# Performance work log

Hardware: AMD Instinct MI355X
Metric: run time of the kernel (lower is better)

Reference implementation:

```python
import jax, jax.numpy as jnp
import numpy as np

V = 400000
D = 16  # max_degree
EPS = 1e-6


def setup_inputs() -> dict:
    key = jax.random.key(0)
    k1, k2, k3, k4 = jax.random.split(key, 4)
    new_verts_coords = jax.random.normal(k1, (V, 3), dtype=jnp.float32)
    verts_src = jax.random.normal(k2, (V, 3), dtype=jnp.float32)
    neighborhood_indices = jax.random.randint(k3, (V, D), 0, V, dtype=jnp.int64)
    neighborhood_weights = jax.random.uniform(k4, (V, D), dtype=jnp.float32)
    return {
        "new_verts_coords": new_verts_coords,
        "verts_src": verts_src,
        "neighborhood_indices": neighborhood_indices,
        "neighborhood_weights": neighborhood_weights,
    }


def reference(new_verts_coords, verts_src, neighborhood_indices, neighborhood_weights):
    # Gather neighbor coords and center at each vertex: (V, D, 3)
    nb_src = verts_src[neighborhood_indices] - verts_src[:, None, :]
    nb_trg = new_verts_coords[neighborhood_indices] - new_verts_coords[:, None, :]

    # Per-vertex cross-covariance 3x3 (Procrustes), regularized as in original
    XtY = jnp.einsum('vdi,vdj->vij', nb_src, nb_trg) + EPS * jnp.eye(3, dtype=nb_src.dtype)

    # Batched tiny SVD; torch.svd returns V (not V^T), R_iT = V @ U^T = (U @ Vh)^T
    U, S, Vh = jnp.linalg.svd(XtY)
    R_iT = jnp.swapaxes(U @ Vh, -1, -2)  # (V, 3, 3)

    # Rotate source neighborhoods and compare to target: (V, D, 3)
    Y_hat = jnp.einsum('vdi,vij->vdj', nb_src, R_iT)
    diff = jnp.linalg.norm(Y_hat - nb_trg, axis=-1)  # (V, D)

    loss_rigid = (diff * neighborhood_weights).sum() / (neighborhood_weights.sum() + EPS)
    return loss_rigid
```

## Files before the change

kernel.cpp:

```cpp
#include <hip/hip_runtime.h>
#include <hip/hip_fp16.h>
#include <math.h>

#define NV   400000
#define DEG  16
#define BLK  256
#define NBLK ((NV + BLK - 1) / BLK)

#define PARTS_OFF  0
#define PACKED_OFF 16384

typedef int   iv4 __attribute__((ext_vector_type(4)));
typedef float fv4 __attribute__((ext_vector_type(4)));
typedef unsigned int uv3 __attribute__((ext_vector_type(3)));

__device__ __forceinline__ float2 h2f2(unsigned int u) {
    union { unsigned int u; __half2 h; } c; c.u = u;
    return __half22float2(c.h);
}

__global__ __launch_bounds__(BLK) void pack_kernel(
    const float* __restrict__ trg_pts, const float* __restrict__ src_pts,
    uv3* __restrict__ packed)
{
    const int v = blockIdx.x * BLK + threadIdx.x;
    if (v >= NV) return;
    float sx = __builtin_nontemporal_load(src_pts + 3 * v + 0);
    float sy = __builtin_nontemporal_load(src_pts + 3 * v + 1);
    float sz = __builtin_nontemporal_load(src_pts + 3 * v + 2);
    float tx = __builtin_nontemporal_load(trg_pts + 3 * v + 0);
    float ty = __builtin_nontemporal_load(trg_pts + 3 * v + 1);
    float tz = __builtin_nontemporal_load(trg_pts + 3 * v + 2);
    union { __half2 h; unsigned int u; } c0, c1, c2;
    c0.h = __floats2half2_rn(sx, sy);
    c1.h = __floats2half2_rn(sz, tx);
    c2.h = __floats2half2_rn(ty, tz);
    uv3 r; r.x = c0.u; r.y = c1.u; r.z = c2.u;
    packed[v] = r;
}

__device__ __forceinline__ void unpack6(uv3 r, float& sx, float& sy, float& sz,
                                        float& tx, float& ty, float& tz)
{
    float2 p0 = h2f2(r.x), p1 = h2f2(r.y), p2 = h2f2(r.z);
    sx = p0.x; sy = p0.y; sz = p1.x; tx = p1.y; ty = p2.x; tz = p2.y;
}

template<int P, int Q, int R>
__device__ __forceinline__ void jrot(float S[3][3], float Vm[3][3]) {
    float apq = S[P][Q];
    float app = S[P][P], aqq = S[Q][Q];
    if (fabsf(apq) > 1e-12f * (fabsf(app) + fabsf(aqq))) {
        float tau = (aqq - app) / (2.0f * apq);
        float t   = (tau >= 0.0f ? 1.0f : -1.0f) / (fabsf(tau) + sqrtf(1.0f + tau * tau));
        float c   = 1.0f / sqrtf(1.0f + t * t);
        float s   = t * c;
        float arp = S[R][P], arq = S[R][Q];
        S[P][P] = app - t * apq;
        S[Q][Q] = aqq + t * apq;
        S[P][Q] = 0.0f; S[Q][P] = 0.0f;
        float nrp = c * arp - s * arq;
        float nrq = s * arp + c * arq;
        S[R][P] = nrp; S[P][R] = nrp;
        S[R][Q] = nrq; S[Q][R] = nrq;
        #pragma unroll
        for (int r = 0; r < 3; ++r) {
            float vp = Vm[r][P], vq = Vm[r][Q];
            Vm[r][P] = c * vp - s * vq;
            Vm[r][Q] = s * vp + c * vq;
        }
    }
}

__global__ __launch_bounds__(BLK) void rigid_loss_kernel(
    const uv3*   __restrict__ packed,
    const int*   __restrict__ nb_idx,
    const float* __restrict__ nb_w,
    float2* __restrict__ block_out)
{
    const int v = blockIdx.x * BLK + threadIdx.x;
    float num = 0.0f, den = 0.0f;

    if (v < NV) {
        int nb[DEG];
        const iv4* idx4 = (const iv4*)(nb_idx + (size_t)v * DEG);
        #pragma unroll
        for (int q = 0; q < 4; ++q) {
            iv4 ti = __builtin_nontemporal_load(idx4 + q);
            nb[4 * q + 0] = ti.x; nb[4 * q + 1] = ti.y; nb[4 * q + 2] = ti.z; nb[4 * q + 3] = ti.w;
        }

        uv3 g[DEG];
        #pragma unroll
        for (int d = 0; d < DEG; ++d) g[d] = packed[nb[d]];

        float s0x, s0y, s0z, t0x, t0y, t0z;
        unpack6(packed[v], s0x, s0y, s0z, t0x, t0y, t0z);

        float A00 = 0, A01 = 0, A02 = 0, A10 = 0, A11 = 0, A12 = 0, A20 = 0, A21 = 0, A22 = 0;
        #pragma unroll
        for (int d = 0; d < DEG; ++d) {
            float sx, sy, sz, tx, ty, tz;
            unpack6(g[d], sx, sy, sz, tx, ty, tz);
            sx -= s0x; sy -= s0y; sz -= s0z;
            tx -= t0x; ty -= t0y; tz -= t0z;
            A00 += sx * tx; A01 += sx * ty; A02 += sx * tz;
            A10 += sy * tx; A11 += sy * ty; A12 += sy * tz;
            A20 += sz * tx; A21 += sz * ty; A22 += sz * tz;
        }
        A00 += 1e-6f; A11 += 1e-6f; A22 += 1e-6f;

        float S[3][3];
        S[0][0] = A00 * A00 + A10 * A10 + A20 * A20;
        S[1][1] = A01 * A01 + A11 * A11 + A21 * A21;
        S[2][2] = A02 * A02 + A12 * A12 + A22 * A22;
        S[0][1] = A00 * A01 + A10 * A11 + A20 * A21; S[1][0] = S[0][1];
        S[0][2] = A00 * A02 + A10 * A12 + A20 * A22; S[2][0] = S[0][2];
        S[1][2] = A01 * A02 + A11 * A12 + A21 * A22; S[2][1] = S[1][2];

        float Vm[3][3] = {{1, 0, 0}, {0, 1, 0}, {0, 0, 1}};
        #pragma unroll
        for (int sweep = 0; sweep < 4; ++sweep) {
            jrot<0, 1, 2>(S, Vm);
            jrot<0, 2, 1>(S, Vm);
            jrot<1, 2, 0>(S, Vm);
        }

        float Qm[3][3] = {{0, 0, 0}, {0, 0, 0}, {0, 0, 0}};
        #pragma unroll
        for (int i = 0; i < 3; ++i) {
            float vx = Vm[0][i], vy = Vm[1][i], vz = Vm[2][i];
            float ux = A00 * vx + A01 * vy + A02 * vz;
            float uy = A10 * vx + A11 * vy + A12 * vz;
            float uz = A20 * vx + A21 * vy + A22 * vz;
            float inv = rsqrtf(fmaxf(ux * ux + uy * uy + uz * uz, 1e-24f));
            ux *= inv; uy *= inv; uz *= inv;
            Qm[0][0] += ux * vx; Qm[0][1] += ux * vy; Qm[0][2] += ux * vz;
            Qm[1][0] += uy * vx; Qm[1][1] += uy * vy; Qm[1][2] += uy * vz;
            Qm[2][0] += uz * vx; Qm[2][1] += uz * vy; Qm[2][2] += uz * vz;
        }

        const fv4* w4 = (const fv4*)(nb_w + (size_t)v * DEG);
        #pragma unroll
        for (int q = 0; q < 4; ++q) {
            fv4 tw = __builtin_nontemporal_load(w4 + q);
            float wl[4] = {tw.x, tw.y, tw.z, tw.w};
            #pragma unroll
            for (int k = 0; k < 4; ++k) {
                const int d = 4 * q + k;
                float sx, sy, sz, tx, ty, tz;
                unpack6(g[d], sx, sy, sz, tx, ty, tz);
                sx -= s0x; sy -= s0y; sz -= s0z;
                tx -= t0x; ty -= t0y; tz -= t0z;
                float yx = Qm[0][0] * sx + Qm[0][1] * sy + Qm[0][2] * sz;
                float yy = Qm[1][0] * sx + Qm[1][1] * sy + Qm[1][2] * sz;
                float yz = Qm[2][0] * sx + Qm[2][1] * sy + Qm[2][2] * sz;
                float dx = yx - tx, dy = yy - ty, dz = yz - tz;
                float dist = sqrtf(dx * dx + dy * dy + dz * dz);
                num += dist * wl[k];
                den += wl[k];
            }
        }
    }

    #pragma unroll
    for (int off = 32; off > 0; off >>= 1) {
        num += __shfl_down(num, off);
        den += __shfl_down(den, off);
    }
    __shared__ float2 wsum[BLK / 64];
    const int lane = threadIdx.x & 63, wid = threadIdx.x >> 6;
    if (lane == 0) wsum[wid] = make_float2(num, den);
    __syncthreads();
    if (threadIdx.x == 0) {
        float2 a = wsum[0];
        #pragma unroll
        for (int i = 1; i < BLK / 64; ++i) { a.x += wsum[i].x; a.y += wsum[i].y; }
        block_out[blockIdx.x] = a;
    }
}

__global__ __launch_bounds__(BLK) void rigid_loss_reduce(
    const float2* __restrict__ parts, float* __restrict__ out)
{
    float num = 0.0f, den = 0.0f;
    for (int i = threadIdx.x; i < NBLK; i += BLK) {
        float2 p = parts[i];
        num += p.x; den += p.y;
    }
    #pragma unroll
    for (int off = 32; off > 0; off >>= 1) {
        num += __shfl_down(num, off);
        den += __shfl_down(den, off);
    }
    __shared__ float2 wsum[BLK / 64];
    const int lane = threadIdx.x & 63, wid = threadIdx.x >> 6;
    if (lane == 0) wsum[wid] = make_float2(num, den);
    __syncthreads();
    if (threadIdx.x == 0) {
        float2 a = wsum[0];
        #pragma unroll
        for (int i = 1; i < BLK / 64; ++i) { a.x += wsum[i].x; a.y += wsum[i].y; }
        out[0] = a.x / (a.y + 1e-6f);
    }
}

extern "C" void kernel_launch(void* const* d_in, const int* in_sizes, int n_in,
                              void* d_out, int out_size, void* d_ws, size_t ws_size,
                              hipStream_t stream) {
    const float* new_verts = (const float*)d_in[0];
    const float* verts_src = (const float*)d_in[1];
    const int*   idx       = (const int*)d_in[2];
    const float* wts       = (const float*)d_in[3];
    float*  out    = (float*)d_out;
    float2* parts  = (float2*)((char*)d_ws + PARTS_OFF);
    uv3*    packed = (uv3*)((char*)d_ws + PACKED_OFF);

    pack_kernel<<<NBLK, BLK, 0, stream>>>(new_verts, verts_src, packed);
    rigid_loss_kernel<<<NBLK, BLK, 0, stream>>>(packed, idx, wts, parts);
    rigid_loss_reduce<<<1, BLK, 0, stream>>>(parts, out);
}
```

Before: 157.7 us.

## Split each vertex across four lanes and use fast intrinsics in Jacobi SVD

The main kernel now assigns four threads per vertex. Each thread gathers four neighbors, and the partial covariance sums are combined with xor shuffles. This raises memory-level parallelism and cuts per-thread register pressure for the random gathers. Every lane in a quad then repeats the 3x3 eigen-solve, so that arithmetic is done four times over. The Jacobi step is also made branchless with hardware rcp/rsq/sqrt approximations, and the sweep count drops from four to three, which risks accuracy.

```diff
diff --git a/kernel.cpp b/kernel.cpp
--- a/kernel.cpp
+++ b/kernel.cpp
@@ -5,10 +5,11 @@
 #define NV   400000
 #define DEG  16
 #define BLK  256
-#define NBLK ((NV + BLK - 1) / BLK)
+#define NBLK_PACK ((NV + BLK - 1) / BLK)
+#define NBLK_MAIN ((NV * 4) / BLK)
 
 #define PARTS_OFF  0
-#define PACKED_OFF 16384
+#define PACKED_OFF 65536
 
 typedef int   iv4 __attribute__((ext_vector_type(4)));
 typedef float fv4 __attribute__((ext_vector_type(4)));
@@ -50,25 +51,24 @@
 __device__ __forceinline__ void jrot(float S[3][3], float Vm[3][3]) {
     float apq = S[P][Q];
     float app = S[P][P], aqq = S[Q][Q];
-    if (fabsf(apq) > 1e-12f * (fabsf(app) + fabsf(aqq))) {
-        float tau = (aqq - app) / (2.0f * apq);
-        float t   = (tau >= 0.0f ? 1.0f : -1.0f) / (fabsf(tau) + sqrtf(1.0f + tau * tau));
-        float c   = 1.0f / sqrtf(1.0f + t * t);
-        float s   = t * c;
-        float arp = S[R][P], arq = S[R][Q];
-        S[P][P] = app - t * apq;
-        S[Q][Q] = aqq + t * apq;
-        S[P][Q] = 0.0f; S[Q][P] = 0.0f;
-        float nrp = c * arp - s * arq;
-        float nrq = s * arp + c * arq;
-        S[R][P] = nrp; S[P][R] = nrp;
-        S[R][Q] = nrq; S[Q][R] = nrq;
-        #pragma unroll
-        for (int r = 0; r < 3; ++r) {
-            float vp = Vm[r][P], vq = Vm[r][Q];
-            Vm[r][P] = c * vp - s * vq;
-            Vm[r][Q] = s * vp + c * vq;
-        }
+    float tau = (aqq - app) * 0.5f * __builtin_amdgcn_rcpf(apq + 1e-30f);
+    float t   = (tau >= 0.0f ? 1.0f : -1.0f) *
+                __builtin_amdgcn_rcpf(fabsf(tau) + __builtin_amdgcn_sqrtf(1.0f + tau * tau));
+    float c   = __builtin_amdgcn_rsqf(1.0f + t * t);
+    float s   = t * c;
+    float arp = S[R][P], arq = S[R][Q];
+    S[P][P] = app - t * apq;
+    S[Q][Q] = aqq + t * apq;
+    S[P][Q] = 0.0f; S[Q][P] = 0.0f;
+    float nrp = c * arp - s * arq;
+    float nrq = s * arp + c * arq;
+    S[R][P] = nrp; S[P][R] = nrp;
+    S[R][Q] = nrq; S[Q][R] = nrq;
+    #pragma unroll
+    for (int r = 0; r < 3; ++r) {
+        float vp = Vm[r][P], vq = Vm[r][Q];
+        Vm[r][P] = c * vp - s * vq;
+        Vm[r][Q] = s * vp + c * vq;
     }
 }
 
@@ -78,89 +78,85 @@
     const float* __restrict__ nb_w,
     float2* __restrict__ block_out)
 {
-    const int v = blockIdx.x * BLK + threadIdx.x;
+    const int tid = blockIdx.x * BLK + threadIdx.x;
+    const int v   = tid >> 2;
+    const int sub = threadIdx.x & 3;
+
+    iv4 ti = __builtin_nontemporal_load(
+        (const iv4*)(nb_idx + (size_t)v * DEG + sub * 4));
+
+    uv3 g[4];
+    g[0] = packed[ti.x]; g[1] = packed[ti.y]; g[2] = packed[ti.z]; g[3] = packed[ti.w];
+
+    float s0x, s0y, s0z, t0x, t0y, t0z;
+    unpack6(packed[v], s0x, s0y, s0z, t0x, t0y, t0z);
+
+    float A00 = 0, A01 = 0, A02 = 0, A10 = 0, A11 = 0, A12 = 0, A20 = 0, A21 = 0, A22 = 0;
+    #pragma unroll
+    for (int k = 0; k < 4; ++k) {
+        float sx, sy, sz, tx, ty, tz;
+        unpack6(g[k], sx, sy, sz, tx, ty, tz);
+        sx -= s0x; sy -= s0y; sz -= s0z;
+        tx -= t0x; ty -= t0y; tz -= t0z;
+        A00 += sx * tx; A01 += sx * ty; A02 += sx * tz;
+        A10 += sy * tx; A11 += sy * ty; A12 += sy * tz;
+        A20 += sz * tx; A21 += sz * ty; A22 += sz * tz;
+    }
+
+    #define QRED(x) x += __shfl_xor(x, 1); x += __shfl_xor(x, 2);
+    QRED(A00) QRED(A01) QRED(A02)
+    QRED(A10) QRED(A11) QRED(A12)
+    QRED(A20) QRED(A21) QRED(A22)
+    #undef QRED
+    A00 += 1e-6f; A11 += 1e-6f; A22 += 1e-6f;
+
+    float S[3][3];
+    S[0][0] = A00 * A00 + A10 * A10 + A20 * A20;
+    S[1][1] = A01 * A01 + A11 * A11 + A21 * A21;
+    S[2][2] = A02 * A02 + A12 * A12 + A22 * A22;
+    S[0][1] = A00 * A01 + A10 * A11 + A20 * A21; S[1][0] = S[0][1];
+    S[0][2] = A00 * A02 + A10 * A12 + A20 * A22; S[2][0] = S[0][2];
+    S[1][2] = A01 * A02 + A11 * A12 + A21 * A22; S[2][1] = S[1][2];
+
+    float Vm[3][3] = {{1, 0, 0}, {0, 1, 0}, {0, 0, 1}};
+    #pragma unroll
+    for (int sweep = 0; sweep < 3; ++sweep) {
+        jrot<0, 1, 2>(S, Vm);
+        jrot<0, 2, 1>(S, Vm);
+        jrot<1, 2, 0>(S, Vm);
+    }
+
+    float Qm[3][3] = {{0, 0, 0}, {0, 0, 0}, {0, 0, 0}};
+    #pragma unroll
+    for (int i = 0; i < 3; ++i) {
+        float vx = Vm[0][i], vy = Vm[1][i], vz = Vm[2][i];
+        float ux = A00 * vx + A01 * vy + A02 * vz;
+        float uy = A10 * vx + A11 * vy + A12 * vz;
+        float uz = A20 * vx + A21 * vy + A22 * vz;
+        float inv = __builtin_amdgcn_rsqf(fmaxf(ux * ux + uy * uy + uz * uz, 1e-24f));
+        ux *= inv; uy *= inv; uz *= inv;
+        Qm[0][0] += ux * vx; Qm[0][1] += ux * vy; Qm[0][2] += ux * vz;
+        Qm[1][0] += uy * vx; Qm[1][1] += uy * vy; Qm[1][2] += uy * vz;
+        Qm[2][0] += uz * vx; Qm[2][1] += uz * vy; Qm[2][2] += uz * vz;
+    }
+
     float num = 0.0f, den = 0.0f;
-
-    if (v < NV) {
-        int nb[DEG];
-        const iv4* idx4 = (const iv4*)(nb_idx + (size_t)v * DEG);
-        #pragma unroll
-        for (int q = 0; q < 4; ++q) {
-            iv4 ti = __builtin_nontemporal_load(idx4 + q);
-            nb[4 * q + 0] = ti.x; nb[4 * q + 1] = ti.y; nb[4 * q + 2] = ti.z; nb[4 * q + 3] = ti.w;
-        }
-
-        uv3 g[DEG];
-        #pragma unroll
-        for (int d = 0; d < DEG; ++d) g[d] = packed[nb[d]];
-
-        float s0x, s0y, s0z, t0x, t0y, t0z;
-        unpack6(packed[v], s0x, s0y, s0z, t0x, t0y, t0z);
-
-        float A00 = 0, A01 = 0, A02 = 0, A10 = 0, A11 = 0, A12 = 0, A20 = 0, A21 = 0, A22 = 0;
-        #pragma unroll
-        for (int d = 0; d < DEG; ++d) {
-            float sx, sy, sz, tx, ty, tz;
-            unpack6(g[d], sx, sy, sz, tx, ty, tz);
-            sx -= s0x; sy -= s0y; sz -= s0z;
-            tx -= t0x; ty -= t0y; tz -= t0z;
-            A00 += sx * tx; A01 += sx * ty; A02 += sx * tz;
-            A10 += sy * tx; A11 += sy * ty; A12 += sy * tz;
-            A20 += sz * tx; A21 += sz * ty; A22 += sz * tz;
-        }
-        A00 += 1e-6f; A11 += 1e-6f; A22 += 1e-6f;
-
-        float S[3][3];
-        S[0][0] = A00 * A00 + A10 * A10 + A20 * A20;
-        S[1][1] = A01 * A01 + A11 * A11 + A21 * A21;
-        S[2][2] = A02 * A02 + A12 * A12 + A22 * A22;
-        S[0][1] = A00 * A01 + A10 * A11 + A20 * A21; S[1][0] = S[0][1];
-        S[0][2] = A00 * A02 + A10 * A12 + A20 * A22; S[2][0] = S[0][2];
-        S[1][2] = A01 * A02 + A11 * A12 + A21 * A22; S[2][1] = S[1][2];
-
-        float Vm[3][3] = {{1, 0, 0}, {0, 1, 0}, {0, 0, 1}};
-        #pragma unroll
-        for (int sweep = 0; sweep < 4; ++sweep) {
-            jrot<0, 1, 2>(S, Vm);
-            jrot<0, 2, 1>(S, Vm);
-            jrot<1, 2, 0>(S, Vm);
-        }
-
-        float Qm[3][3] = {{0, 0, 0}, {0, 0, 0}, {0, 0, 0}};
-        #pragma unroll
-        for (int i = 0; i < 3; ++i) {
-            float vx = Vm[0][i], vy = Vm[1][i], vz = Vm[2][i];
-            float ux = A00 * vx + A01 * vy + A02 * vz;
-            float uy = A10 * vx + A11 * vy + A12 * vz;
-            float uz = A20 * vx + A21 * vy + A22 * vz;
-            float inv = rsqrtf(fmaxf(ux * ux + uy * uy + uz * uz, 1e-24f));
-            ux *= inv; uy *= inv; uz *= inv;
-            Qm[0][0] += ux * vx; Qm[0][1] += ux * vy; Qm[0][2] += ux * vz;
-            Qm[1][0] += uy * vx; Qm[1][1] += uy * vy; Qm[1][2] += uy * vz;
-            Qm[2][0] += uz * vx; Qm[2][1] += uz * vy; Qm[2][2] += uz * vz;
-        }
-
-        const fv4* w4 = (const fv4*)(nb_w + (size_t)v * DEG);
-        #pragma unroll
-        for (int q = 0; q < 4; ++q) {
-            fv4 tw = __builtin_nontemporal_load(w4 + q);
-            float wl[4] = {tw.x, tw.y, tw.z, tw.w};
-            #pragma unroll
-            for (int k = 0; k < 4; ++k) {
-                const int d = 4 * q + k;
-                float sx, sy, sz, tx, ty, tz;
-                unpack6(g[d], sx, sy, sz, tx, ty, tz);
-                sx -= s0x; sy -= s0y; sz -= s0z;
-                tx -= t0x; ty -= t0y; tz -= t0z;
-                float yx = Qm[0][0] * sx + Qm[0][1] * sy + Qm[0][2] * sz;
-                float yy = Qm[1][0] * sx + Qm[1][1] * sy + Qm[1][2] * sz;
-                float yz = Qm[2][0] * sx + Qm[2][1] * sy + Qm[2][2] * sz;
-                float dx = yx - tx, dy = yy - ty, dz = yz - tz;
-                float dist = sqrtf(dx * dx + dy * dy + dz * dz);
-                num += dist * wl[k];
-                den += wl[k];
-            }
-        }
+    fv4 tw = __builtin_nontemporal_load(
+        (const fv4*)(nb_w + (size_t)v * DEG + sub * 4));
+    float wl[4] = {tw.x, tw.y, tw.z, tw.w};
+    #pragma unroll
+    for (int k = 0; k < 4; ++k) {
+        float sx, sy, sz, tx, ty, tz;
+        unpack6(g[k], sx, sy, sz, tx, ty, tz);
+        sx -= s0x; sy -= s0y; sz -= s0z;
+        tx -= t0x; ty -= t0y; tz -= t0z;
+        float yx = Qm[0][0] * sx + Qm[0][1] * sy + Qm[0][2] * sz;
+        float yy = Qm[1][0] * sx + Qm[1][1] * sy + Qm[1][2] * sz;
+        float yz = Qm[2][0] * sx + Qm[2][1] * sy + Qm[2][2] * sz;
+        float dx = yx - tx, dy = yy - ty, dz = yz - tz;
+        float dist = __builtin_amdgcn_sqrtf(dx * dx + dy * dy + dz * dz);
+        num += dist * wl[k];
+        den += wl[k];
     }
 
     #pragma unroll
@@ -184,7 +180,7 @@
     const float2* __restrict__ parts, float* __restrict__ out)
 {
     float num = 0.0f, den = 0.0f;
-    for (int i = threadIdx.x; i < NBLK; i += BLK) {
+    for (int i = threadIdx.x; i < NBLK_MAIN; i += BLK) {
         float2 p = parts[i];
         num += p.x; den += p.y;
     }
@@ -216,7 +212,7 @@
     float2* parts  = (float2*)((char*)d_ws + PARTS_OFF);
     uv3*    packed = (uv3*)((char*)d_ws + PACKED_OFF);
 
-    pack_kernel<<<NBLK, BLK, 0, stream>>>(new_verts, verts_src, packed);
-    rigid_loss_kernel<<<NBLK, BLK, 0, stream>>>(packed, idx, wts, parts);
+    pack_kernel<<<NBLK_PACK, BLK, 0, stream>>>(new_verts, verts_src, packed);
+    rigid_loss_kernel<<<NBLK_MAIN, BLK, 0, stream>>>(packed, idx, wts, parts);
     rigid_loss_reduce<<<1, BLK, 0, stream>>>(parts, out);
 }
```

New measurement: 149.1 us. 1.06x faster.
